# Kernel optimization log

Measured on AMD Instinct MI355X. Metric: run time of the kernel, lower is better.

The kernel has to match this reference:

```python
import jax, jax.numpy as jnp
import numpy as np

N, E, D, H = 50000, 500000, 128, 8
DH = D // H  # per-head dim = int(out_dim // num_heads)
EPS_LN = 1e-5
EPS_BN = 1e-5


def _ln(x, g, b):
    m = x.mean(-1, keepdims=True)
    v = ((x - m) ** 2).mean(-1, keepdims=True)
    return (x - m) * jax.lax.rsqrt(v + EPS_LN) * g + b


def _bn(x, g, b):
    # BatchNorm1d, training-mode statistics (biased variance over the batch)
    m = x.mean(0)
    v = ((x - m) ** 2).mean(0)
    return (x - m) * jax.lax.rsqrt(v + EPS_BN) * g + b


def setup_inputs() -> dict:
    key = jax.random.key(0)
    ks = jax.random.split(key, 16)
    rn = lambda k, shape: (jax.random.normal(k, shape, jnp.float32) * 0.05)
    h = jax.random.normal(ks[0], (N, D), jnp.float32)
    src = jax.random.randint(ks[1], (E,), 0, N).astype(jnp.int32)
    # guarantee every node receives at least one message so z > 0 (no 0/0)
    dst = jnp.concatenate([jnp.arange(N, dtype=jnp.int32),
                           jax.random.randint(ks[2], (E - N,), 0, N).astype(jnp.int32)])
    return {
        "h": h, "src": src, "dst": dst,
        # per-node TransformerEncoder (seq_len == 1 subgraphs)
        "Win": rn(ks[3], (3 * D, D)), "bin": jnp.zeros((3 * D,), jnp.float32),
        "Wout": rn(ks[4], (D, D)), "bout": jnp.zeros((D,), jnp.float32),
        "Wte1": rn(ks[5], (4 * D, D)), "bte1": jnp.zeros((4 * D,), jnp.float32),
        "Wte2": rn(ks[6], (D, 4 * D)), "bte2": jnp.zeros((D,), jnp.float32),
        "ln1g": jnp.ones((D,), jnp.float32), "ln1b": jnp.zeros((D,), jnp.float32),
        "ln2g": jnp.ones((D,), jnp.float32), "ln2b": jnp.zeros((D,), jnp.float32),
        # graph multi-head attention projections (use_bias=False)
        "WQ": rn(ks[7], (D, D)), "WK": rn(ks[8], (D, D)), "WV": rn(ks[9], (D, D)),
        # node-wise FFN + batch norms
        "W1": rn(ks[10], (2 * D, D)), "b1": jnp.zeros((2 * D,), jnp.float32),
        "W2": rn(ks[11], (D, 2 * D)), "b2": jnp.zeros((D,), jnp.float32),
        "bn1g": jnp.ones((D,), jnp.float32), "bn1b": jnp.zeros((D,), jnp.float32),
        "bn2g": jnp.ones((D,), jnp.float32), "bn2b": jnp.zeros((D,), jnp.float32),
    }


def _forward(h, src, dst, Win, bin_, Wout, bout, Wte1, bte1, Wte2, bte2,
             ln1g, ln1b, ln2g, ln2b, WQ, WK, WV,
             W1, b1, W2, b2, bn1g, bn1b, bn2g, bn2b):
    # --- per-node TransformerEncoder. Each dgl.node_subgraph(g, [i]) contains
    # only the center node, so self-attention runs over a length-1 sequence:
    # softmax of a single score is 1, hence attn_out = out_proj(v).
    v = h @ Win[2 * D:].T + bin_[2 * D:]            # V slice of in_proj
    x = _ln(h + (v @ Wout.T + bout), ln1g, ln1b)
    ff = jax.nn.relu(x @ Wte1.T + bte1) @ Wte2.T + bte2
    hsub = _ln(x + ff, ln2g, ln2b)                  # [N, D]

    # --- graph multi-head attention (DGL apply_edges / send_and_recv)
    Qh = (hsub @ WQ.T).reshape(N, H, DH)
    Kh = (hsub @ WK.T).reshape(N, H, DH)
    Vh = (hsub @ WV.T).reshape(N, H, DH)
    score = (Kh[src] * Qh[dst]).sum(-1)             # [E, H]  K_src . Q_dst
    score = jnp.exp(jnp.clip(score / np.sqrt(DH), -5.0, 5.0))
    wV = jax.ops.segment_sum(Vh[src] * score[:, :, None], dst, num_segments=N)
    z = jax.ops.segment_sum(score, dst, num_segments=N)
    attn = (wV / z[:, :, None]).reshape(N, D)

    # --- residual + BN + FFN + residual + BN (dropout p=0 / eval mode)
    hh = _bn(hsub + attn, bn1g, bn1b)
    h_in2 = hh
    hh = jax.nn.relu(hh @ W1.T + b1) @ W2.T + b2
    return _bn(h_in2 + hh, bn2g, bn2b)


def reference(h, src, dst, Win, bin, Wout, bout, Wte1, bte1, Wte2, bte2,
              ln1g, ln1b, ln2g, ln2b, WQ, WK, WV,
              W1, b1, W2, b2, bn1g, bn1b, bn2g, bn2b):
    return _forward(h, src, dst, Win, bin, Wout, bout, Wte1, bte1, Wte2, bte2,
                    ln1g, ln1b, ln2g, ln2b, WQ, WK, WV,
                    W1, b1, W2, b2, bn1g, bn1b, bn2g, bn2b)
```

## Files before the change

### kernel.cpp

```cpp
#include <hip/hip_runtime.h>
#include <hip/hip_bf16.h>


#define D_ 128

typedef __attribute__((ext_vector_type(8))) short short8;
typedef __attribute__((ext_vector_type(4))) short short4v;
typedef __attribute__((ext_vector_type(4))) float f32x4;

__device__ __forceinline__ float b2f(ushort u) {
    union { uint u32; float f; } x; x.u32 = ((uint)u) << 16; return x.f;
}
__device__ __forceinline__ ushort f2b(float f) {
    union { __hip_bfloat16 h; ushort u; } v; v.h = __float2bfloat16(f); return v.u;
}

template<int AMODE, int EPI, bool RELU, bool RESF32>
__global__ __launch_bounds__(512) void gemm_bf16(
    const void* __restrict__ Aptr, const ushort* __restrict__ W,
    const float* __restrict__ bias, void* __restrict__ C,
    const float* __restrict__ bn_in, float* __restrict__ bn_out,
    const float* __restrict__ bng, const float* __restrict__ bnb,
    const void* __restrict__ resid, const ushort* __restrict__ y1res,
    const float* __restrict__ lng, const float* __restrict__ lnb,
    float invn, int n, int K, int M)
{
    __shared__ ushort Abuf[2][128 * 32];
    __shared__ ushort Bbuf[2][128 * 32];
    __shared__ float s_sh[128], t_sh[128];

    const int t    = threadIdx.x;
    const int lane = t & 63;
    const int w    = t >> 6;
    const int r0   = blockIdx.x * 128;
    const int c0   = blockIdx.y * 128;
    const int wr   = (w >> 1) * 32;
    const int wc   = (w & 1) * 64;
    const int rl   = lane & 15;
    const int kh   = lane >> 4;

    if (AMODE == 2 || EPI == 2) {
        if (t < 128) {
            float m   = bn_in[t] * invn;
            float var = bn_in[128 + t] * invn - m * m;
            float rs  = rsqrtf(var + 1e-5f);
            float s   = rs * bng[t];
            s_sh[t] = s;
            t_sh[t] = bnb[t] - m * s;
        }
        __syncthreads();
    }

    f32x4 acc[2][4] = {};
    const int nc = K >> 5;
    const int row = t >> 2, pos = t & 3;

    if (AMODE == 1) {
        for (int c = 0; c < nc; ++c) {
            int kc = c * 32;
            const int ch = pos;
            int gr = r0 + row;
            short8 aval = {};
            if (gr < n) {
                const float* Af = (const float*)Aptr;
                float4 f0 = *reinterpret_cast<const float4*>(Af + (size_t)gr * K + kc + ch * 8);
                float4 f1 = *reinterpret_cast<const float4*>(Af + (size_t)gr * K + kc + ch * 8 + 4);
                aval[0] = (short)f2b(f0.x); aval[1] = (short)f2b(f0.y);
                aval[2] = (short)f2b(f0.z); aval[3] = (short)f2b(f0.w);
                aval[4] = (short)f2b(f1.x); aval[5] = (short)f2b(f1.y);
                aval[6] = (short)f2b(f1.z); aval[7] = (short)f2b(f1.w);
            }
            short8 bval = *reinterpret_cast<const short8*>(W + (size_t)(c0 + row) * K + kc + ch * 8);
            __syncthreads();
            int sw = ch ^ ((row >> 1) & 3);
            *reinterpret_cast<short8*>(&Abuf[0][row * 32 + sw * 8]) = aval;
            *reinterpret_cast<short8*>(&Bbuf[0][row * 32 + sw * 8]) = bval;
            __syncthreads();
            short8 af[2], bfr[4];
            #pragma unroll
            for (int m = 0; m < 2; ++m) {
                int rr = wr + m * 16 + rl;
                af[m] = *reinterpret_cast<const short8*>(&Abuf[0][rr * 32 + (kh ^ ((rr >> 1) & 3)) * 8]);
            }
            #pragma unroll
            for (int nn = 0; nn < 4; ++nn) {
                int col = wc + nn * 16 + rl;
                bfr[nn] = *reinterpret_cast<const short8*>(&Bbuf[0][col * 32 + (kh ^ ((col >> 1) & 3)) * 8]);
            }
            #pragma unroll
            for (int m = 0; m < 2; ++m)
                #pragma unroll
                for (int nn = 0; nn < 4; ++nn)
                    acc[m][nn] = __builtin_amdgcn_mfma_f32_16x16x32_bf16(
                        bfr[nn], af[m], acc[m][nn], 0, 0, 0);
        }
    } else {
        const int ch = pos ^ ((row >> 1) & 3);
        const ushort* Abase = (const ushort*)Aptr + (size_t)(r0 + row) * K + ch * 8;
        const ushort* Bbase = W + (size_t)(c0 + row) * K + ch * 8;
        __builtin_amdgcn_global_load_lds(
            (const __attribute__((address_space(1))) void*)Abase,
            (__attribute__((address_space(3))) void*)&Abuf[0][t * 8], 16, 0, 0);
        __builtin_amdgcn_global_load_lds(
            (const __attribute__((address_space(1))) void*)Bbase,
            (__attribute__((address_space(3))) void*)&Bbuf[0][t * 8], 16, 0, 0);
        __syncthreads();
        for (int c = 0; c < nc; ++c) {
            if (c + 1 < nc) {
                int half = (c + 1) & 1;
                __builtin_amdgcn_global_load_lds(
                    (const __attribute__((address_space(1))) void*)(Abase + (c + 1) * 32),
                    (__attribute__((address_space(3))) void*)&Abuf[half][t * 8], 16, 0, 0);
                __builtin_amdgcn_global_load_lds(
                    (const __attribute__((address_space(1))) void*)(Bbase + (c + 1) * 32),
                    (__attribute__((address_space(3))) void*)&Bbuf[half][t * 8], 16, 0, 0);
            }
            const int cur = c & 1;
            const int kc  = c * 32;
            short8 af[2], bfr[4];
            #pragma unroll
            for (int m = 0; m < 2; ++m) {
                int rr = wr + m * 16 + rl;
                af[m] = *reinterpret_cast<const short8*>(&Abuf[cur][rr * 32 + (kh ^ ((rr >> 1) & 3)) * 8]);
            }
            if (AMODE == 2) {
                #pragma unroll
                for (int m = 0; m < 2; ++m) {
                    short8 v = af[m];
                    #pragma unroll
                    for (int q = 0; q < 8; ++q) {
                        int cch = kc + kh * 8 + q;
                        v[q] = (short)f2b(fmaf(b2f((ushort)v[q]), s_sh[cch], t_sh[cch]));
                    }
                    af[m] = v;
                }
            }
            #pragma unroll
            for (int nn = 0; nn < 4; ++nn) {
                int col = wc + nn * 16 + rl;
                bfr[nn] = *reinterpret_cast<const short8*>(&Bbuf[cur][col * 32 + (kh ^ ((col >> 1) & 3)) * 8]);
            }
            #pragma unroll
            for (int m = 0; m < 2; ++m)
                #pragma unroll
                for (int nn = 0; nn < 4; ++nn)
                    acc[m][nn] = __builtin_amdgcn_mfma_f32_16x16x32_bf16(
                        bfr[nn], af[m], acc[m][nn], 0, 0, 0);
            __syncthreads();
        }
    }

    const int ch4 = kh * 4;

    if (EPI == 1) {
        __shared__ float lnS[128][2], lnS2[128][2];
        float4 bb[4];
        #pragma unroll
        for (int nn = 0; nn < 4; ++nn)
            bb[nn] = *reinterpret_cast<const float4*>(bias + wc + nn * 16 + ch4);
        #pragma unroll
        for (int m = 0; m < 2; ++m) {
            int r = r0 + wr + m * 16 + rl;
            float s = 0.f, s2 = 0.f;
            #pragma unroll
            for (int nn = 0; nn < 4; ++nn) {
                int c = wc + nn * 16 + ch4;
                float rv[4] = {0.f, 0.f, 0.f, 0.f};
                if (r < n) {
                    if (RESF32) {
                        float4 f = *reinterpret_cast<const float4*>((const float*)resid + (size_t)r * 128 + c);
                        rv[0] = f.x; rv[1] = f.y; rv[2] = f.z; rv[3] = f.w;
                    } else {
                        short4v f = *reinterpret_cast<const short4v*>((const ushort*)resid + (size_t)r * 128 + c);
                        rv[0] = b2f((ushort)f[0]); rv[1] = b2f((ushort)f[1]);
                        rv[2] = b2f((ushort)f[2]); rv[3] = b2f((ushort)f[3]);
                    }
                }
                float bj[4] = {bb[nn].x, bb[nn].y, bb[nn].z, bb[nn].w};
                #pragma unroll
                for (int j = 0; j < 4; ++j) {
                    float o = acc[m][nn][j] + bj[j] + rv[j];
                    acc[m][nn][j] = o;
                    s += o; s2 += o * o;
                }
            }
            s  += __shfl_xor(s, 16);  s  += __shfl_xor(s, 32);
            s2 += __shfl_xor(s2, 16); s2 += __shfl_xor(s2, 32);
            if (kh == 0) {
                lnS[wr + m * 16 + rl][w & 1]  = s;
                lnS2[wr + m * 16 + rl][w & 1] = s2;
            }
        }
        __syncthreads();
        #pragma unroll
        for (int m = 0; m < 2; ++m) {
            int rloc = wr + m * 16 + rl;
            int r = r0 + rloc;
            float S  = lnS[rloc][0] + lnS[rloc][1];
            float S2 = lnS2[rloc][0] + lnS2[rloc][1];
            float mean = S * (1.f / 128.f);
            float var  = S2 * (1.f / 128.f) - mean * mean;
            float rs   = rsqrtf(var + 1e-5f);
            if (r >= n) continue;
            #pragma unroll
            for (int nn = 0; nn < 4; ++nn) {
                int c = wc + nn * 16 + ch4;
                float4 gv = *reinterpret_cast<const float4*>(lng + c);
                float4 bv = *reinterpret_cast<const float4*>(lnb + c);
                float gj[4] = {gv.x, gv.y, gv.z, gv.w};
                float bj[4] = {bv.x, bv.y, bv.z, bv.w};
                short4v p;
                #pragma unroll
                for (int j = 0; j < 4; ++j)
                    p[j] = (short)f2b((acc[m][nn][j] - mean) * rs * gj[j] + bj[j]);
                *reinterpret_cast<short4v*>((ushort*)C + (size_t)r * 128 + c) = p;
            }
        }
        return;
    }

    if (EPI == 2) {
        __shared__ float csum[128], csum2[128];
        if (t < 128) { csum[t] = 0.f; csum2[t] = 0.f; }
        __syncthreads();
        float ps[4][4] = {};
        float ps2[4][4] = {};
        #pragma unroll
        for (int m = 0; m < 2; ++m) {
            int r = r0 + wr + m * 16 + rl;
            bool ok = r < n;
            #pragma unroll
            for (int nn = 0; nn < 4; ++nn) {
                int c = wc + nn * 16 + ch4;
                float4 bb = *reinterpret_cast<const float4*>(bias + c);
                float bj[4] = {bb.x, bb.y, bb.z, bb.w};
                short4v yv = {};
                if (ok) yv = *reinterpret_cast<const short4v*>(y1res + (size_t)r * 128 + c);
                short4v p;
                #pragma unroll
                for (int j = 0; j < 4; ++j) {
                    float o = 0.f;
                    if (ok) {
                        o = acc[m][nn][j] + bj[j]
                          + fmaf(b2f((ushort)yv[j]), s_sh[c + j], t_sh[c + j]);
                    }
                    ps[nn][j] += o; ps2[nn][j] += o * o;
                    p[j] = (short)f2b(o);
                }
                if (ok)
                    *reinterpret_cast<short4v*>((ushort*)C + (size_t)r * 128 + c) = p;
            }
        }
        #pragma unroll
        for (int nn = 0; nn < 4; ++nn)
            #pragma unroll
            for (int j = 0; j < 4; ++j) {
                float a = ps[nn][j], b = ps2[nn][j];
                #pragma unroll
                for (int o2 = 1; o2 < 16; o2 <<= 1) {
                    a += __shfl_xor(a, o2);
                    b += __shfl_xor(b, o2);
                }
                if (rl == 0) {
                    int c = wc + nn * 16 + ch4 + j;
                    atomicAdd(&csum[c], a);
                    atomicAdd(&csum2[c], b);
                }
            }
        __syncthreads();
        if (t < 128) {
            atomicAdd(bn_out + t, csum[t]);
            atomicAdd(bn_out + 128 + t, csum2[t]);
        }
        return;
    }

    #pragma unroll
    for (int m = 0; m < 2; ++m) {
        int r = r0 + wr + m * 16 + rl;
        if (r >= n) continue;
        #pragma unroll
        for (int nn = 0; nn < 4; ++nn) {
            int c = c0 + wc + nn * 16 + ch4;
            f32x4 vacc = acc[m][nn];
            float4 bb = make_float4(0.f, 0.f, 0.f, 0.f);
            if (bias) bb = *reinterpret_cast<const float4*>(bias + c);
            float o0 = vacc[0] + bb.x, o1 = vacc[1] + bb.y;
            float o2 = vacc[2] + bb.z, o3 = vacc[3] + bb.w;
            if (RELU) {
                o0 = fmaxf(o0, 0.f); o1 = fmaxf(o1, 0.f);
                o2 = fmaxf(o2, 0.f); o3 = fmaxf(o3, 0.f);
            }
            short4v p;
            p[0] = (short)f2b(o0); p[1] = (short)f2b(o1);
            p[2] = (short)f2b(o2); p[3] = (short)f2b(o3);
            *reinterpret_cast<short4v*>((ushort*)C + (size_t)r * M + c) = p;
        }
    }
}

__global__ __launch_bounds__(512) void ffn_ln_kernel(
    const ushort* __restrict__ X,   const ushort* __restrict__ W1g,
    const ushort* __restrict__ W2g,
    const float* __restrict__ b1v,  const float* __restrict__ b2v,
    const float* __restrict__ lng,  const float* __restrict__ lnb,
    ushort* __restrict__ out, int n)
{
    __shared__ ushort Xs[128 * 128];
    __shared__ ushort FF1[128 * 64];
    __shared__ ushort W1s[2][64 * 128];
    __shared__ ushort W2s[2][128 * 64];
    __shared__ float lnS[128][2], lnS2[128][2];

    const int t    = threadIdx.x;
    const int lane = t & 63;
    const int w    = t >> 6;
    const int r0   = blockIdx.x * 128;
    const int rl   = lane & 15;
    const int kh   = lane >> 4;
    const int wr   = (w >> 1) * 32;
    const int wc1  = (w & 1) * 32;
    const int wc2  = (w & 1) * 64;

    #pragma unroll
    for (int i = 0; i < 4; ++i) {
        int s = t + i * 512;
        int row = s >> 4, pos = s & 15;
        int srcch = pos ^ ((row >> 1) & 7);
        if (r0 + row < n)
            __builtin_amdgcn_global_load_lds(
                (const __attribute__((address_space(1))) void*)(X + (size_t)(r0 + row) * 128 + srcch * 8),
                (__attribute__((address_space(3))) void*)&Xs[s * 8], 16, 0, 0);
    }
    #pragma unroll
    for (int i = 0; i < 2; ++i) {
        int s = t + i * 512;
        int row = s >> 4, pos = s & 15;
        int srcch = pos ^ ((row >> 1) & 7);
        __builtin_amdgcn_global_load_lds(
            (const __attribute__((address_space(1))) void*)(W1g + (size_t)row * 128 + srcch * 8),
            (__attribute__((address_space(3))) void*)&W1s[0][s * 8], 16, 0, 0);
    }
    #pragma unroll
    for (int i = 0; i < 2; ++i) {
        int s = t + i * 512;
        int row = s >> 3, pos = s & 7;
        int srcch = pos ^ ((row >> 1) & 7);
        __builtin_amdgcn_global_load_lds(
            (const __attribute__((address_space(1))) void*)(W2g + (size_t)row * 512 + srcch * 8),
            (__attribute__((address_space(3))) void*)&W2s[0][s * 8], 16, 0, 0);
    }
    __syncthreads();

    f32x4 acc2[2][4] = {};

    for (int c = 0; c < 8; ++c) {
        const int cur = c & 1, nxt = cur ^ 1;
        if (c < 7) {
            #pragma unroll
            for (int i = 0; i < 2; ++i) {
                int s = t + i * 512;
                int row = s >> 4, pos = s & 15;
                int srcch = pos ^ ((row >> 1) & 7);
                __builtin_amdgcn_global_load_lds(
                    (const __attribute__((address_space(1))) void*)(W1g + (size_t)((c + 1) * 64 + row) * 128 + srcch * 8),
                    (__attribute__((address_space(3))) void*)&W1s[nxt][s * 8], 16, 0, 0);
            }
            #pragma unroll
            for (int i = 0; i < 2; ++i) {
                int s = t + i * 512;
                int row = s >> 3, pos = s & 7;
                int srcch = pos ^ ((row >> 1) & 7);
                __builtin_amdgcn_global_load_lds(
                    (const __attribute__((address_space(1))) void*)(W2g + (size_t)row * 512 + (c + 1) * 64 + srcch * 8),
                    (__attribute__((address_space(3))) void*)&W2s[nxt][s * 8], 16, 0, 0);
            }
        }
        f32x4 acc1[2][2] = {};
        #pragma unroll
        for (int ks = 0; ks < 4; ++ks) {
            short8 af[2], bf[2];
            #pragma unroll
            for (int m = 0; m < 2; ++m) {
                int row = wr + m * 16 + rl;
                int chn = ks * 4 + kh;
                af[m] = *reinterpret_cast<const short8*>(&Xs[row * 128 + (chn ^ ((row >> 1) & 7)) * 8]);
            }
            #pragma unroll
            for (int nn = 0; nn < 2; ++nn) {
                int colL = wc1 + nn * 16 + rl;
                int chn = ks * 4 + kh;
                bf[nn] = *reinterpret_cast<const short8*>(&W1s[cur][colL * 128 + (chn ^ ((colL >> 1) & 7)) * 8]);
            }
            #pragma unroll
            for (int m = 0; m < 2; ++m)
                #pragma unroll
                for (int nn = 0; nn < 2; ++nn)
                    acc1[m][nn] = __builtin_amdgcn_mfma_f32_16x16x32_bf16(
                        bf[nn], af[m], acc1[m][nn], 0, 0, 0);
        }
        #pragma unroll
        for (int m = 0; m < 2; ++m) {
            int row = wr + m * 16 + rl;
            #pragma unroll
            for (int nn = 0; nn < 2; ++nn) {
                int colL = wc1 + nn * 16 + kh * 4;
                float4 bb = *reinterpret_cast<const float4*>(b1v + c * 64 + colL);
                short4v p;
                p[0] = (short)f2b(fmaxf(acc1[m][nn][0] + bb.x, 0.f));
                p[1] = (short)f2b(fmaxf(acc1[m][nn][1] + bb.y, 0.f));
                p[2] = (short)f2b(fmaxf(acc1[m][nn][2] + bb.z, 0.f));
                p[3] = (short)f2b(fmaxf(acc1[m][nn][3] + bb.w, 0.f));
                int chn = colL >> 3;
                *reinterpret_cast<short4v*>(
                    &FF1[row * 64 + (chn ^ ((row >> 1) & 7)) * 8 + (kh & 1) * 4]) = p;
            }
        }
        __syncthreads();

        #pragma unroll
        for (int ks = 0; ks < 2; ++ks) {
            short8 af[2], bf[4];
            #pragma unroll
            for (int m = 0; m < 2; ++m) {
                int row = wr + m * 16 + rl;
                int chn = ks * 4 + kh;
                af[m] = *reinterpret_cast<const short8*>(&FF1[row * 64 + (chn ^ ((row >> 1) & 7)) * 8]);
            }
            #pragma unroll
            for (int nn = 0; nn < 4; ++nn) {
                int col = wc2 + nn * 16 + rl;
                int chn = ks * 4 + kh;
                bf[nn] = *reinterpret_cast<const short8*>(&W2s[cur][col * 64 + (chn ^ ((col >> 1) & 7)) * 8]);
            }
            #pragma unroll
            for (int m = 0; m < 2; ++m)
                #pragma unroll
                for (int nn = 0; nn < 4; ++nn)
                    acc2[m][nn] = __builtin_amdgcn_mfma_f32_16x16x32_bf16(
                        bf[nn], af[m], acc2[m][nn], 0, 0, 0);
        }
        __syncthreads();
    }

    const int ch4 = kh * 4;
    #pragma unroll
    for (int m = 0; m < 2; ++m) {
        int rloc = wr + m * 16 + rl;
        float s = 0.f, s2 = 0.f;
        #pragma unroll
        for (int nn = 0; nn < 4; ++nn) {
            int col = wc2 + nn * 16 + ch4;
            int chn = col >> 3;
            short4v xv = *reinterpret_cast<const short4v*>(
                &Xs[rloc * 128 + (chn ^ ((rloc >> 1) & 7)) * 8 + (kh & 1) * 4]);
            float4 bb = *reinterpret_cast<const float4*>(b2v + col);
            float bj[4] = {bb.x, bb.y, bb.z, bb.w};
            #pragma unroll
            for (int j = 0; j < 4; ++j) {
                float o = acc2[m][nn][j] + bj[j] + b2f((ushort)xv[j]);
                acc2[m][nn][j] = o;
                s += o; s2 += o * o;
            }
        }
        s  += __shfl_xor(s, 16);  s  += __shfl_xor(s, 32);
        s2 += __shfl_xor(s2, 16); s2 += __shfl_xor(s2, 32);
        if (kh == 0) {
            lnS[rloc][w & 1]  = s;
            lnS2[rloc][w & 1] = s2;
        }
    }
    __syncthreads();
    #pragma unroll
    for (int m = 0; m < 2; ++m) {
        int rloc = wr + m * 16 + rl;
        int r = r0 + rloc;
        float S  = lnS[rloc][0] + lnS[rloc][1];
        float S2 = lnS2[rloc][0] + lnS2[rloc][1];
        float mean = S * (1.f / 128.f);
        float var  = S2 * (1.f / 128.f) - mean * mean;
        float rs   = rsqrtf(var + 1e-5f);
        if (r >= n) continue;
        #pragma unroll
        for (int nn = 0; nn < 4; ++nn) {
            int col = wc2 + nn * 16 + ch4;
            float4 gv = *reinterpret_cast<const float4*>(lng + col);
            float4 bv = *reinterpret_cast<const float4*>(lnb + col);
            float gj[4] = {gv.x, gv.y, gv.z, gv.w};
            float bj[4] = {bv.x, bv.y, bv.z, bv.w};
            short4v p;
            #pragma unroll
            for (int j = 0; j < 4; ++j)
                p[j] = (short)f2b((acc2[m][nn][j] - mean) * rs * gj[j] + bj[j]);
            *reinterpret_cast<short4v*>(out + (size_t)r * 128 + col) = p;
        }
    }
}

__global__ __launch_bounds__(256) void zero_kernel(int4* __restrict__ p, int n4)
{
    int i = blockIdx.x * blockDim.x + threadIdx.x;
    int stride = gridDim.x * blockDim.x;
    int4 z = make_int4(0, 0, 0, 0);
    for (; i < n4; i += stride) p[i] = z;
}

__global__ void hist_kernel(const int* __restrict__ dst, int* __restrict__ cnt, int E_)
{
    int e = blockIdx.x * blockDim.x + threadIdx.x;
    if (e < E_) atomicAdd(cnt + dst[e], 1);
}

__global__ __launch_bounds__(256) void scan_block_kernel(
    int* __restrict__ data, int* __restrict__ bsum, int n)
{
    __shared__ int tmp[256];
    int i = blockIdx.x * 256 + threadIdx.x;
    int v = (i < n) ? data[i] : 0;
    tmp[threadIdx.x] = v;
    __syncthreads();
    #pragma unroll
    for (int o = 1; o < 256; o <<= 1) {
        int y = (threadIdx.x >= o) ? tmp[threadIdx.x - o] : 0;
        __syncthreads();
        tmp[threadIdx.x] += y;
        __syncthreads();
    }
    if (i < n) data[i] = tmp[threadIdx.x] - v;
    if (threadIdx.x == 255) bsum[blockIdx.x] = tmp[255];
}

__global__ __launch_bounds__(256) void add_off_kernel(
    int* __restrict__ data, const int* __restrict__ bsum, int n, int nb)
{
    __shared__ int red[4];
    int b = blockIdx.x;
    int v = (threadIdx.x < b && threadIdx.x < nb) ? bsum[threadIdx.x] : 0;
    #pragma unroll
    for (int o = 1; o < 64; o <<= 1) v += __shfl_xor(v, o);
    if ((threadIdx.x & 63) == 0) red[threadIdx.x >> 6] = v;
    __syncthreads();
    int off = red[0] + red[1] + red[2] + red[3];
    int i = b * 256 + threadIdx.x;
    if (i < n) data[i] += off;
}

__global__ void scatter_kernel(const int* __restrict__ src, const int* __restrict__ dst,
                               int* __restrict__ rowptr, int* __restrict__ csr_src, int E_)
{
    int e = blockIdx.x * blockDim.x + threadIdx.x;
    if (e >= E_) return;
    int pos = atomicAdd(rowptr + dst[e], 1);
    csr_src[pos] = src[e];
}

__global__ __launch_bounds__(256) void attn_agg_kernel(
    const int* __restrict__ rowptr, const int* __restrict__ csr_src,
    const ushort* __restrict__ QKV, const ushort* __restrict__ hsub,
    ushort* __restrict__ out, int n)
{
    int node  = (blockIdx.x * blockDim.x + threadIdx.x) >> 5;
    int lane5 = threadIdx.x & 31;
    int slot  = lane5 >> 3;
    int hd    = lane5 & 7;
    bool valid = node < n;
    int nd = valid ? node : 0;
    int start = (valid && nd) ? rowptr[nd - 1] : 0;
    int end   = valid ? rowptr[nd] : 0;

    const ushort* qp = QKV + (size_t)nd * 384 + hd * 16;
    short8 q0 = *reinterpret_cast<const short8*>(qp);
    short8 q1 = *reinterpret_cast<const short8*>(qp + 8);
    float q[16];
    #pragma unroll
    for (int i = 0; i < 8; ++i) { q[i] = b2f((ushort)q0[i]); q[8 + i] = b2f((ushort)q1[i]); }

    float acc[16] = {};
    float zh = 0.f;
    for (int j = start; j < end; j += 4) {
        int idx = j + slot;
        if (idx < end) {
            int s = csr_src[idx];
            const ushort* kp = QKV + (size_t)s * 384 + 128 + hd * 16;
            short8 k0 = *reinterpret_cast<const short8*>(kp);
            short8 k1 = *reinterpret_cast<const short8*>(kp + 8);
            float p = 0.f;
            #pragma unroll
            for (int i = 0; i < 8; ++i) {
                p = fmaf(b2f((ushort)k0[i]), q[i], p);
                p = fmaf(b2f((ushort)k1[i]), q[8 + i], p);
            }
            float sc = __expf(fminf(fmaxf(p * 0.25f, -5.f), 5.f));
            short8 v0 = *reinterpret_cast<const short8*>(kp + 128);
            short8 v1 = *reinterpret_cast<const short8*>(kp + 136);
            #pragma unroll
            for (int i = 0; i < 8; ++i) {
                acc[i]     = fmaf(sc, b2f((ushort)v0[i]), acc[i]);
                acc[8 + i] = fmaf(sc, b2f((ushort)v1[i]), acc[8 + i]);
            }
            zh += sc;
        }
    }
    #pragma unroll
    for (int i = 0; i < 16; ++i) {
        acc[i] += __shfl_xor(acc[i], 8);
        acc[i] += __shfl_xor(acc[i], 16);
    }
    zh += __shfl_xor(zh, 8);
    zh += __shfl_xor(zh, 16);

    if (slot == 0 && valid) {
        const ushort* hp = hsub + (size_t)nd * D_ + hd * 16;
        short8 h0 = *reinterpret_cast<const short8*>(hp);
        short8 h1 = *reinterpret_cast<const short8*>(hp + 8);
        float inv = 1.f / zh;
        short8 o0, o1;
        #pragma unroll
        for (int i = 0; i < 8; ++i) {
            o0[i] = (short)f2b(b2f((ushort)h0[i]) + acc[i] * inv);
            o1[i] = (short)f2b(b2f((ushort)h1[i]) + acc[8 + i] * inv);
        }
        ushort* op = out + (size_t)nd * D_ + hd * 16;
        *reinterpret_cast<short8*>(op)     = o0;
        *reinterpret_cast<short8*>(op + 8) = o1;
    }
}

__global__ __launch_bounds__(256) void bn_stats_kernel(
    const ushort* __restrict__ x, float* __restrict__ sums, int n)
{
    int c    = threadIdx.x & 127;
    int half = threadIdx.x >> 7;
    float s = 0.f, s2 = 0.f;
    for (int r = blockIdx.x * 2 + half; r < n; r += gridDim.x * 2) {
        float v = b2f(x[(size_t)r * D_ + c]);
        s += v; s2 += v * v;
    }
    __shared__ float ls[256], ls2[256];
    ls[threadIdx.x] = s; ls2[threadIdx.x] = s2;
    __syncthreads();
    if (half == 0) {
        s  += ls[threadIdx.x + 128];
        s2 += ls2[threadIdx.x + 128];
        atomicAdd(sums + c, s);
        atomicAdd(sums + 128 + c, s2);
    }
}

__global__ void bn_norm_kernel(const ushort* __restrict__ x,
                               const float* __restrict__ stats,
                               const float* __restrict__ g, const float* __restrict__ b,
                               float* __restrict__ out, float invn, int total4)
{
    int i = blockIdx.x * blockDim.x + threadIdx.x;
    if (i >= total4) return;
    int cb = (i << 2) & 127;
    short4v v = reinterpret_cast<const short4v*>(x)[i];
    float4 o;
    float r[4];
    #pragma unroll
    for (int q = 0; q < 4; ++q) {
        int c = cb + q;
        float m   = stats[c] * invn;
        float var = stats[128 + c] * invn - m * m;
        float rs  = rsqrtf(var + 1e-5f);
        r[q] = (b2f((ushort)v[q]) - m) * rs * g[c] + b[c];
    }
    o.x = r[0]; o.y = r[1]; o.z = r[2]; o.w = r[3];
    reinterpret_cast<float4*>(out)[i] = o;
}

struct WPtrs { const float* p[7]; };

__global__ __launch_bounds__(256) void prep_w_kernel(
    const float* __restrict__ Win, const float* __restrict__ bin_,
    const float* __restrict__ Wout, const float* __restrict__ bout,
    WPtrs wp, ushort* __restrict__ wbf, float* __restrict__ bfused)
{
    int b = blockIdx.x;
    if (b < 64) {
        int idx = b * 256 + threadIdx.x;
        int i = idx >> 7, c = idx & 127;
        const float* WinV = Win + 256 * 128;
        float s = 0.f;
        for (int j = 0; j < 128; ++j)
            s = fmaf(Wout[i * 128 + j], WinV[j * 128 + c], s);
        wbf[245760 + idx] = f2b(s);
        if (c == 0) {
            float tb = bout[i];
            for (int j = 0; j < 128; ++j)
                tb = fmaf(Wout[i * 128 + j], bin_[256 + j], tb);
            bfused[i] = tb;
        }
    } else {
        const int off[8] = {0, 65536, 131072, 147456, 163840, 180224, 212992, 245760};
        int e0 = ((b - 64) * 256 + threadIdx.x) * 4;
        if (e0 >= 245760) return;
        int s = 0;
        #pragma unroll
        for (int j = 1; j < 7; ++j) if (e0 >= off[j]) s = j;
        float4 f = *reinterpret_cast<const float4*>(wp.p[s] + (e0 - off[s]));
        short4v o;
        o[0] = (short)f2b(f.x); o[1] = (short)f2b(f.y);
        o[2] = (short)f2b(f.z); o[3] = (short)f2b(f.w);
        *reinterpret_cast<short4v*>(wbf + e0) = o;
    }
}

extern "C" void kernel_launch(void* const* d_in, const int* in_sizes, int n_in,
                              void* d_out, int out_size, void* d_ws, size_t ws_size,
                              hipStream_t stream)
{
    const float* h    = (const float*)d_in[0];
    const int*   src  = (const int*)d_in[1];
    const int*   dst  = (const int*)d_in[2];
    const float* Win  = (const float*)d_in[3];
    const float* bin_ = (const float*)d_in[4];
    const float* Wout = (const float*)d_in[5];
    const float* bout = (const float*)d_in[6];
    const float* Wte1 = (const float*)d_in[7];
    const float* bte1 = (const float*)d_in[8];
    const float* Wte2 = (const float*)d_in[9];
    const float* bte2 = (const float*)d_in[10];
    const float* ln1g = (const float*)d_in[11];
    const float* ln1b = (const float*)d_in[12];
    const float* ln2g = (const float*)d_in[13];
    const float* ln2b = (const float*)d_in[14];
    const float* WQ   = (const float*)d_in[15];
    const float* WK   = (const float*)d_in[16];
    const float* WV   = (const float*)d_in[17];
    const float* W1   = (const float*)d_in[18];
    const float* b1   = (const float*)d_in[19];
    const float* W2   = (const float*)d_in[20];
    const float* b2   = (const float*)d_in[21];
    const float* bn1g = (const float*)d_in[22];
    const float* bn1b = (const float*)d_in[23];
    const float* bn2g = (const float*)d_in[24];
    const float* bn2b = (const float*)d_in[25];

    const int N_ = in_sizes[0] / D_;
    const int E_ = in_sizes[1];
    const size_t S2 = (size_t)N_ * D_ / 2;

    float* ws = (float*)d_ws;
    size_t off_tail = 7 * S2;
    size_t need = (off_tail + 131072 + 128 + 512) * sizeof(float)
                + (size_t)(N_ + E_ + 256) * sizeof(int) + 4096;
    if (ws_size < need) return;

    ushort* bufA   = (ushort*)ws;
    ushort* bufB   = (ushort*)(ws + S2);
    ushort* bufC   = (ushort*)(ws + 2 * S2);
    ushort* bufD   = (ushort*)(ws + 3 * S2);
    ushort* wbf    = (ushort*)(ws + off_tail);
    float*  bfused = ws + off_tail + 131072;
    float*  stats  = bfused + 128;
    int* rowptr  = (int*)(stats + 512);
    int* csr_src = rowptr + N_;
    int* bsum    = csr_src + E_;

    const ushort* Wte1_bf = wbf;
    const ushort* Wte2_bf = wbf + 65536;
    const ushort* WQKV_bf = wbf + 131072;
    const ushort* W1_bf   = wbf + 180224;
    const ushort* W2_bf   = wbf + 212992;
    ushort*       Wf_bf   = wbf + 245760;

    dim3 blk(256);
    dim3 blk512(512);
    const int rowBlocks = (N_ + 127) / 128;
    const int totElems  = N_ * D_;
    const dim3 gNode((N_ + 7) / 8);
    const int nb = (N_ + 255) / 256;
    const float invn = 1.f / (float)N_;

    {
        int n4 = (512 + N_) / 4;
        int zblocks = (n4 + 255) / 256;
        if (zblocks > 128) zblocks = 128;
        zero_kernel<<<dim3(zblocks), blk, 0, stream>>>((int4*)stats, n4);
    }

    hist_kernel<<<dim3((E_ + 255) / 256), blk, 0, stream>>>(dst, rowptr, E_);
    scan_block_kernel<<<dim3(nb), blk, 0, stream>>>(rowptr, bsum, N_);
    add_off_kernel<<<dim3(nb), blk, 0, stream>>>(rowptr, bsum, N_, nb);
    scatter_kernel<<<dim3((E_ + 255) / 256), blk, 0, stream>>>(src, dst, rowptr, csr_src, E_);

    WPtrs wp;
    wp.p[0] = Wte1; wp.p[1] = Wte2; wp.p[2] = WQ; wp.p[3] = WK; wp.p[4] = WV;
    wp.p[5] = W1;   wp.p[6] = W2;
    prep_w_kernel<<<dim3(304), blk, 0, stream>>>(Win, bin_, Wout, bout, wp, wbf, bfused);

    gemm_bf16<1, 1, false, true><<<dim3(rowBlocks, 1), blk512, 0, stream>>>(
        h, Wf_bf, bfused, bufA, nullptr, nullptr, nullptr, nullptr,
        h, nullptr, ln1g, ln1b, 0.f, N_, 128, 128);
    ffn_ln_kernel<<<dim3(rowBlocks), blk512, 0, stream>>>(
        bufA, Wte1_bf, Wte2_bf, bte1, bte2, ln2g, ln2b, bufC, N_);

    gemm_bf16<0, 0, false, false><<<dim3(rowBlocks, 3), blk512, 0, stream>>>(
        bufC, WQKV_bf, nullptr, bufD, nullptr, nullptr, nullptr, nullptr,
        nullptr, nullptr, nullptr, nullptr, 0.f, N_, 128, 384);
    attn_agg_kernel<<<gNode, blk, 0, stream>>>(
        rowptr, csr_src, bufD, bufC, bufA, N_);

    bn_stats_kernel<<<dim3(512), blk, 0, stream>>>(bufA, stats, N_);

    gemm_bf16<2, 0, true, false><<<dim3(rowBlocks, 2), blk512, 0, stream>>>(
        bufA, W1_bf, b1, bufD, stats, nullptr, bn1g, bn1b,
        nullptr, nullptr, nullptr, nullptr, invn, N_, 128, 256);
    gemm_bf16<0, 2, false, false><<<dim3(rowBlocks, 1), blk512, 0, stream>>>(
        bufD, W2_bf, b2, bufB, stats, stats + 256, bn1g, bn1b,
        nullptr, bufA, nullptr, nullptr, invn, N_, 256, 128);
    bn_norm_kernel<<<dim3((totElems / 4 + 255) / 256), blk, 0, stream>>>(
        bufB, stats + 256, bn2g, bn2b, (float*)d_out, invn, totElems / 4);
}
```

Baseline: 257.9 us.

## Single-buffer FFN weight tiles and alias LN scratch into FF1 to cut LDS

The fused FFN+LayerNorm kernel drops double-buffering of the W1/W2 weight chunks: each iteration loads its chunk and synchronises before computing. The LayerNorm partial-sum scratch now reuses the FF1 buffer instead of its own arrays. Together these shrink LDS from about 98KB to about 64KB per block so more blocks can be resident per CU, at the cost of exposing weight-load latency on every chunk. It also changes the half-offset index used for the FF1 store and the Xs residual read from (kh&1) to ((col>>2)&1), which gives the same value here since col includes kh*4.

```diff
diff --git a/kernel.cpp b/kernel.cpp
--- a/kernel.cpp
+++ b/kernel.cpp
@@ -308,9 +308,8 @@
 {
     __shared__ ushort Xs[128 * 128];
     __shared__ ushort FF1[128 * 64];
-    __shared__ ushort W1s[2][64 * 128];
-    __shared__ ushort W2s[2][128 * 64];
-    __shared__ float lnS[128][2], lnS2[128][2];
+    __shared__ ushort W1s[64 * 128];
+    __shared__ ushort W2s[128 * 64];
 
     const int t    = threadIdx.x;
     const int lane = t & 63;
@@ -332,50 +331,31 @@
                 (const __attribute__((address_space(1))) void*)(X + (size_t)(r0 + row) * 128 + srcch * 8),
                 (__attribute__((address_space(3))) void*)&Xs[s * 8], 16, 0, 0);
     }
-    #pragma unroll
-    for (int i = 0; i < 2; ++i) {
-        int s = t + i * 512;
-        int row = s >> 4, pos = s & 15;
-        int srcch = pos ^ ((row >> 1) & 7);
-        __builtin_amdgcn_global_load_lds(
-            (const __attribute__((address_space(1))) void*)(W1g + (size_t)row * 128 + srcch * 8),
-            (__attribute__((address_space(3))) void*)&W1s[0][s * 8], 16, 0, 0);
-    }
-    #pragma unroll
-    for (int i = 0; i < 2; ++i) {
-        int s = t + i * 512;
-        int row = s >> 3, pos = s & 7;
-        int srcch = pos ^ ((row >> 1) & 7);
-        __builtin_amdgcn_global_load_lds(
-            (const __attribute__((address_space(1))) void*)(W2g + (size_t)row * 512 + srcch * 8),
-            (__attribute__((address_space(3))) void*)&W2s[0][s * 8], 16, 0, 0);
-    }
     __syncthreads();
 
     f32x4 acc2[2][4] = {};
 
     for (int c = 0; c < 8; ++c) {
-        const int cur = c & 1, nxt = cur ^ 1;
-        if (c < 7) {
-            #pragma unroll
-            for (int i = 0; i < 2; ++i) {
-                int s = t + i * 512;
-                int row = s >> 4, pos = s & 15;
-                int srcch = pos ^ ((row >> 1) & 7);
-                __builtin_amdgcn_global_load_lds(
-                    (const __attribute__((address_space(1))) void*)(W1g + (size_t)((c + 1) * 64 + row) * 128 + srcch * 8),
-                    (__attribute__((address_space(3))) void*)&W1s[nxt][s * 8], 16, 0, 0);
-            }
-            #pragma unroll
-            for (int i = 0; i < 2; ++i) {
-                int s = t + i * 512;
-                int row = s >> 3, pos = s & 7;
-                int srcch = pos ^ ((row >> 1) & 7);
-                __builtin_amdgcn_global_load_lds(
-                    (const __attribute__((address_space(1))) void*)(W2g + (size_t)row * 512 + (c + 1) * 64 + srcch * 8),
-                    (__attribute__((address_space(3))) void*)&W2s[nxt][s * 8], 16, 0, 0);
-            }
-        }
+        #pragma unroll
+        for (int i = 0; i < 2; ++i) {
+            int s = t + i * 512;
+            int row = s >> 4, pos = s & 15;
+            int srcch = pos ^ ((row >> 1) & 7);
+            __builtin_amdgcn_global_load_lds(
+                (const __attribute__((address_space(1))) void*)(W1g + (size_t)(c * 64 + row) * 128 + srcch * 8),
+                (__attribute__((address_space(3))) void*)&W1s[s * 8], 16, 0, 0);
+        }
+        #pragma unroll
+        for (int i = 0; i < 2; ++i) {
+            int s = t + i * 512;
+            int row = s >> 3, pos = s & 7;
+            int srcch = pos ^ ((row >> 1) & 7);
+            __builtin_amdgcn_global_load_lds(
+                (const __attribute__((address_space(1))) void*)(W2g + (size_t)row * 512 + c * 64 + srcch * 8),
+                (__attribute__((address_space(3))) void*)&W2s[s * 8], 16, 0, 0);
+        }
+        __syncthreads();
+
         f32x4 acc1[2][2] = {};
         #pragma unroll
         for (int ks = 0; ks < 4; ++ks) {
@@ -390,7 +370,7 @@
             for (int nn = 0; nn < 2; ++nn) {
                 int colL = wc1 + nn * 16 + rl;
                 int chn = ks * 4 + kh;
-                bf[nn] = *reinterpret_cast<const short8*>(&W1s[cur][colL * 128 + (chn ^ ((colL >> 1) & 7)) * 8]);
+                bf[nn] = *reinterpret_cast<const short8*>(&W1s[colL * 128 + (chn ^ ((colL >> 1) & 7)) * 8]);
             }
             #pragma unroll
             for (int m = 0; m < 2; ++m)
@@ -411,9 +391,9 @@
                 p[1] = (short)f2b(fmaxf(acc1[m][nn][1] + bb.y, 0.f));
                 p[2] = (short)f2b(fmaxf(acc1[m][nn][2] + bb.z, 0.f));
                 p[3] = (short)f2b(fmaxf(acc1[m][nn][3] + bb.w, 0.f));
-                int chn = colL >> 3;
+                int chn = colL >> 3, half = (colL >> 2) & 1;
                 *reinterpret_cast<short4v*>(
-                    &FF1[row * 64 + (chn ^ ((row >> 1) & 7)) * 8 + (kh & 1) * 4]) = p;
+                    &FF1[row * 64 + (chn ^ ((row >> 1) & 7)) * 8 + half * 4]) = p;
             }
         }
         __syncthreads();
@@ -431,7 +411,7 @@
             for (int nn = 0; nn < 4; ++nn) {
                 int col = wc2 + nn * 16 + rl;
                 int chn = ks * 4 + kh;
-                bf[nn] = *reinterpret_cast<const short8*>(&W2s[cur][col * 64 + (chn ^ ((col >> 1) & 7)) * 8]);
+                bf[nn] = *reinterpret_cast<const short8*>(&W2s[col * 64 + (chn ^ ((col >> 1) & 7)) * 8]);
             }
             #pragma unroll
             for (int m = 0; m < 2; ++m)
@@ -443,6 +423,8 @@
         __syncthreads();
     }
 
+    float* lnSf  = (float*)FF1;
+    float* lnS2f = lnSf + 256;
     const int ch4 = kh * 4;
     #pragma unroll
     for (int m = 0; m < 2; ++m) {
@@ -453,7 +435,7 @@
             int col = wc2 + nn * 16 + ch4;
             int chn = col >> 3;
             short4v xv = *reinterpret_cast<const short4v*>(
-                &Xs[rloc * 128 + (chn ^ ((rloc >> 1) & 7)) * 8 + (kh & 1) * 4]);
+                &Xs[rloc * 128 + (chn ^ ((rloc >> 1) & 7)) * 8 + ((col >> 2) & 1) * 4]);
             float4 bb = *reinterpret_cast<const float4*>(b2v + col);
             float bj[4] = {bb.x, bb.y, bb.z, bb.w};
             #pragma unroll
@@ -466,8 +448,8 @@
         s  += __shfl_xor(s, 16);  s  += __shfl_xor(s, 32);
         s2 += __shfl_xor(s2, 16); s2 += __shfl_xor(s2, 32);
         if (kh == 0) {
-            lnS[rloc][w & 1]  = s;
-            lnS2[rloc][w & 1] = s2;
+            lnSf[rloc * 2 + (w & 1)]  = s;
+            lnS2f[rloc * 2 + (w & 1)] = s2;
         }
     }
     __syncthreads();
@@ -475,8 +457,8 @@
     for (int m = 0; m < 2; ++m) {
         int rloc = wr + m * 16 + rl;
         int r = r0 + rloc;
-        float S  = lnS[rloc][0] + lnS[rloc][1];
-        float S2 = lnS2[rloc][0] + lnS2[rloc][1];
+        float S  = lnSf[rloc * 2 + 0] + lnSf[rloc * 2 + 1];
+        float S2 = lnS2f[rloc * 2 + 0] + lnS2f[rloc * 2 + 1];
         float mean = S * (1.f / 128.f);
         float var  = S2 * (1.f / 128.f) - mean * mean;
         float rs   = rsqrtf(var + 1e-5f);
```

After: 252.7 us. -2.0%, faster.
